# Performance work log

Hardware: AMD Instinct MI355X
Metric: run time of the kernel (lower is better)

The kernel has to match this reference:

```python
import jax, jax.numpy as jnp
import numpy as np

N = 1_000_000      # occupied voxels
GRID = 256         # voxel grid extent per axis
K = 27             # 3^3 kernel offsets
CIN, COUT = 2, 16


def _build_nbr_map(coords: np.ndarray) -> np.ndarray:
    """Kernel-offset neighbor map like MinkowskiEngine's kernel map.
    coords: [N,3] unique int voxel coords. Returns [N,K] int32, -1 = no neighbor.
    """
    key = (coords[:, 0] * GRID + coords[:, 1]) * GRID + coords[:, 2]
    order = np.argsort(key)
    skey = key[order]
    offsets = np.array([[dx, dy, dz]
                        for dx in (-1, 0, 1)
                        for dy in (-1, 0, 1)
                        for dz in (-1, 0, 1)], dtype=np.int64)
    nbr = np.full((coords.shape[0], K), -1, dtype=np.int32)
    for k in range(K):
        nc = coords + offsets[k]
        valid = np.all((nc >= 0) & (nc < GRID), axis=1)
        nkey = (nc[:, 0] * GRID + nc[:, 1]) * GRID + nc[:, 2]
        pos = np.clip(np.searchsorted(skey, nkey), 0, coords.shape[0] - 1)
        hit = valid & (skey[pos] == nkey)
        nbr[:, k] = np.where(hit, order[pos].astype(np.int32), -1)
    return nbr


def setup_inputs() -> dict:
    rng = np.random.default_rng(0)
    lin = rng.choice(GRID ** 3, size=N, replace=False)  # unique voxel ids
    coords = np.stack([lin // (GRID * GRID), (lin // GRID) % GRID, lin % GRID],
                      axis=1).astype(np.int64)
    nbr = _build_nbr_map(coords)
    key = jax.random.key(0)
    k1, k2 = jax.random.split(key)
    features = jax.random.normal(k1, (N, CIN), dtype=jnp.float32)
    # MinkowskiConvolution kernel: one [Cin,Cout] matrix per kernel offset, no bias
    kernel = jax.random.normal(k2, (K, CIN, COUT), dtype=jnp.float32) * 0.1
    return {"features": features, "kernel": kernel, "nbr_idx": jnp.asarray(nbr)}


def reference(features, kernel, nbr_idx):
    # gather-GEMM-scatter sparse conv: out[n] = sum_k W_k^T x[nbr(n,k)]
    mask = (nbr_idx >= 0)
    safe = jnp.maximum(nbr_idx, 0)
    gathered = features[safe]                              # [N,K,Cin]
    gathered = gathered * mask[..., None].astype(features.dtype)
    return jnp.einsum('nkc,kcd->nd', gathered, kernel)     # [N,Cout]
```

## Files before the change

### kernel.cpp

```cpp
#include <hip/hip_runtime.h>

#define K_OFF 27
#define CIN   2
#define COUT  16
#define BLK   256
#define CH    9

__global__ __launch_bounds__(BLK) void spconv_gather_kernel(
    const float* __restrict__ feats,
    const float* __restrict__ w,
    const int*   __restrict__ nbr,
    float*       __restrict__ out,
    int n_pts)
{
    __shared__ int s_nbr[BLK * K_OFF];

    const int tid     = threadIdx.x;
    const int lane    = tid & 63;
    const int wv      = tid >> 6;
    const int base_pt = blockIdx.x * BLK;
    const int wpt     = base_pt + wv * 64;

    int* sw = s_nbr + wv * (64 * K_OFF);
    const long long g0         = (long long)wpt * K_OFF;
    const long long total_ints = (long long)n_pts * K_OFF;

    int4*       sw4 = reinterpret_cast<int4*>(sw);
    const int4* g4  = reinterpret_cast<const int4*>(nbr + g0);
    #pragma unroll
    for (int j = 0; j < 7; ++j) {
        const int i = lane + j * 64;
        if (i < (64 * K_OFF) / 4) {
            const long long g = g0 + (long long)i * 4;
            sw4[i] = (g + 3 < total_ints) ? g4[i] : make_int4(-1, -1, -1, -1);
        }
    }
    asm volatile("s_waitcnt lgkmcnt(0)" ::: "memory");
    __builtin_amdgcn_wave_barrier();

    const float2* feats2 = reinterpret_cast<const float2*>(feats);
    const int row = lane * K_OFF;

    auto issue = [&](int kb, float2* f, float* m) {
        #pragma unroll
        for (int j = 0; j < CH; ++j) {
            const int idx = sw[row + kb + j];
            m[j] = (idx >= 0) ? 1.0f : 0.0f;
            f[j] = feats2[idx > 0 ? idx : 0];
        }
    };
    float acc[COUT];
    #pragma unroll
    for (int d = 0; d < COUT; ++d) acc[d] = 0.f;

    auto fma9 = [&](int kb, const float2* f, const float* m) {
        #pragma unroll
        for (int j = 0; j < CH; ++j) {
            const float fx = f[j].x * m[j];
            const float fy = f[j].y * m[j];
            const float* wk = w + (kb + j) * (CIN * COUT);
            #pragma unroll
            for (int d = 0; d < COUT; ++d) {
                acc[d] = fmaf(fx, wk[d],        acc[d]);
                acc[d] = fmaf(fy, wk[COUT + d], acc[d]);
            }
        }
    };

    float2 fA[CH], fB[CH];
    float  mA[CH], mB[CH];
    issue(0,  fA, mA);
    issue(CH, fB, mB);
    fma9(0, fA, mA);
    issue(2 * CH, fA, mA);
    fma9(CH, fB, mB);
    fma9(2 * CH, fA, mA);

    const int n = base_pt + tid;
    if (n < n_pts) {
        float4* o = reinterpret_cast<float4*>(out + (size_t)n * COUT);
        o[0] = make_float4(acc[0],  acc[1],  acc[2],  acc[3]);
        o[1] = make_float4(acc[4],  acc[5],  acc[6],  acc[7]);
        o[2] = make_float4(acc[8],  acc[9],  acc[10], acc[11]);
        o[3] = make_float4(acc[12], acc[13], acc[14], acc[15]);
    }
}

extern "C" void kernel_launch(void* const* d_in, const int* in_sizes, int n_in,
                              void* d_out, int out_size, void* d_ws, size_t ws_size,
                              hipStream_t stream) {
    const float* feats = (const float*)d_in[0];
    const float* w     = (const float*)d_in[1];
    const int*   nbr   = (const int*)d_in[2];
    float*       out   = (float*)d_out;

    const int n_pts = in_sizes[0] / CIN;
    const int grid  = (n_pts + BLK - 1) / BLK;

    spconv_gather_kernel<<<grid, BLK, 0, stream>>>(feats, w, nbr, out, n_pts);
}
```

Baseline: 64.02 us.

## Use persistent waves with register-prefetched neighbor tiles and two-chunk gather

Converts the kernel to a persistent grid capped at 1280 blocks, where each wave loops over 64-point tiles with a stride. It prefetches the next tile's neighbor indices into registers while the current tile is gathered and computed, so the index load overlaps with the feature gathers. The gather is also regrouped from three chunks of 9 into chunks of 14 and 13, which puts more loads in flight at a time. In exchange it raises register pressure and may lower occupancy, and the fixed grid cap may not suit every GPU configuration.

```diff
diff --git a/kernel.cpp b/kernel.cpp
--- a/kernel.cpp
+++ b/kernel.cpp
@@ -4,85 +4,127 @@
 #define CIN   2
 #define COUT  16
 #define BLK   256
-#define CH    9
+#define WAVES 4
+#define IPW   (64 * K_OFF)
+#define I4PW  (IPW / 4)
 
-__global__ __launch_bounds__(BLK) void spconv_gather_kernel(
+__global__ __launch_bounds__(BLK) void spconv_kernel(
     const float* __restrict__ feats,
     const float* __restrict__ w,
     const int*   __restrict__ nbr,
     float*       __restrict__ out,
-    int n_pts)
+    int n_pts, int n_tiles)
 {
-    __shared__ int s_nbr[BLK * K_OFF];
+    __shared__ int s_nbr[WAVES * IPW];
 
-    const int tid     = threadIdx.x;
-    const int lane    = tid & 63;
-    const int wv      = tid >> 6;
-    const int base_pt = blockIdx.x * BLK;
-    const int wpt     = base_pt + wv * 64;
+    const int tid  = threadIdx.x;
+    const int lane = tid & 63;
+    const int wv   = tid >> 6;
+    int* sw = s_nbr + wv * IPW;
+    int4* sw4 = reinterpret_cast<int4*>(sw);
 
-    int* sw = s_nbr + wv * (64 * K_OFF);
-    const long long g0         = (long long)wpt * K_OFF;
     const long long total_ints = (long long)n_pts * K_OFF;
+    const float2* feats2 = reinterpret_cast<const float2*>(feats);
 
-    int4*       sw4 = reinterpret_cast<int4*>(sw);
-    const int4* g4  = reinterpret_cast<const int4*>(nbr + g0);
-    #pragma unroll
-    for (int j = 0; j < 7; ++j) {
-        const int i = lane + j * 64;
-        if (i < (64 * K_OFF) / 4) {
+    const int wstride = gridDim.x * WAVES;
+    int tile = blockIdx.x * WAVES + wv;
+    if (tile >= n_tiles) return;
+
+    int4 r[7];
+    {
+        const long long g0 = (long long)tile * IPW;
+        const int4* g4 = reinterpret_cast<const int4*>(nbr + g0);
+        #pragma unroll
+        for (int j = 0; j < 7; ++j) {
+            const int i = lane + j * 64;
             const long long g = g0 + (long long)i * 4;
-            sw4[i] = (g + 3 < total_ints) ? g4[i] : make_int4(-1, -1, -1, -1);
+            r[j] = (i < I4PW && g + 3 < total_ints) ? g4[i] : make_int4(-1,-1,-1,-1);
         }
     }
-    asm volatile("s_waitcnt lgkmcnt(0)" ::: "memory");
-    __builtin_amdgcn_wave_barrier();
 
-    const float2* feats2 = reinterpret_cast<const float2*>(feats);
-    const int row = lane * K_OFF;
+    while (true) {
+        #pragma unroll
+        for (int j = 0; j < 7; ++j) {
+            const int i = lane + j * 64;
+            if (i < I4PW) sw4[i] = r[j];
+        }
+        asm volatile("s_waitcnt lgkmcnt(0)" ::: "memory");
+        __builtin_amdgcn_sched_barrier(0);
+        __builtin_amdgcn_wave_barrier();
 
-    auto issue = [&](int kb, float2* f, float* m) {
-        #pragma unroll
-        for (int j = 0; j < CH; ++j) {
-            const int idx = sw[row + kb + j];
-            m[j] = (idx >= 0) ? 1.0f : 0.0f;
-            f[j] = feats2[idx > 0 ? idx : 0];
-        }
-    };
-    float acc[COUT];
-    #pragma unroll
-    for (int d = 0; d < COUT; ++d) acc[d] = 0.f;
+        const int cur = tile;
+        tile += wstride;
+        const bool more = (tile < n_tiles);
 
-    auto fma9 = [&](int kb, const float2* f, const float* m) {
-        #pragma unroll
-        for (int j = 0; j < CH; ++j) {
-            const float fx = f[j].x * m[j];
-            const float fy = f[j].y * m[j];
-            const float* wk = w + (kb + j) * (CIN * COUT);
+        if (more) {
+            const long long g0 = (long long)tile * IPW;
+            const int4* g4 = reinterpret_cast<const int4*>(nbr + g0);
             #pragma unroll
-            for (int d = 0; d < COUT; ++d) {
-                acc[d] = fmaf(fx, wk[d],        acc[d]);
-                acc[d] = fmaf(fy, wk[COUT + d], acc[d]);
+            for (int j = 0; j < 7; ++j) {
+                const int i = lane + j * 64;
+                const long long g = g0 + (long long)i * 4;
+                r[j] = (i < I4PW && g + 3 < total_ints) ? g4[i] : make_int4(-1,-1,-1,-1);
             }
         }
-    };
 
-    float2 fA[CH], fB[CH];
-    float  mA[CH], mB[CH];
-    issue(0,  fA, mA);
-    issue(CH, fB, mB);
-    fma9(0, fA, mA);
-    issue(2 * CH, fA, mA);
-    fma9(CH, fB, mB);
-    fma9(2 * CH, fA, mA);
+        float acc[COUT];
+        #pragma unroll
+        for (int d = 0; d < COUT; ++d) acc[d] = 0.f;
+        const int row = lane * K_OFF;
 
-    const int n = base_pt + tid;
-    if (n < n_pts) {
-        float4* o = reinterpret_cast<float4*>(out + (size_t)n * COUT);
-        o[0] = make_float4(acc[0],  acc[1],  acc[2],  acc[3]);
-        o[1] = make_float4(acc[4],  acc[5],  acc[6],  acc[7]);
-        o[2] = make_float4(acc[8],  acc[9],  acc[10], acc[11]);
-        o[3] = make_float4(acc[12], acc[13], acc[14], acc[15]);
+        {
+            float2 f[14]; float m[14];
+            #pragma unroll
+            for (int j = 0; j < 14; ++j) {
+                const int idx = sw[row + j];
+                m[j] = (idx >= 0) ? 1.0f : 0.0f;
+                f[j] = feats2[idx > 0 ? idx : 0];
+            }
+            #pragma unroll
+            for (int j = 0; j < 14; ++j) {
+                const float fx = f[j].x * m[j];
+                const float fy = f[j].y * m[j];
+                const float* wk = w + j * (CIN * COUT);
+                #pragma unroll
+                for (int d = 0; d < COUT; ++d) {
+                    acc[d] = fmaf(fx, wk[d],        acc[d]);
+                    acc[d] = fmaf(fy, wk[COUT + d], acc[d]);
+                }
+            }
+        }
+        {
+            float2 f[13]; float m[13];
+            #pragma unroll
+            for (int j = 0; j < 13; ++j) {
+                const int idx = sw[row + 14 + j];
+                m[j] = (idx >= 0) ? 1.0f : 0.0f;
+                f[j] = feats2[idx > 0 ? idx : 0];
+            }
+            #pragma unroll
+            for (int j = 0; j < 13; ++j) {
+                const float fx = f[j].x * m[j];
+                const float fy = f[j].y * m[j];
+                const float* wk = w + (14 + j) * (CIN * COUT);
+                #pragma unroll
+                for (int d = 0; d < COUT; ++d) {
+                    acc[d] = fmaf(fx, wk[d],        acc[d]);
+                    acc[d] = fmaf(fy, wk[COUT + d], acc[d]);
+                }
+            }
+        }
+
+        const int n = cur * 64 + lane;
+        if (n < n_pts) {
+            float4* o = reinterpret_cast<float4*>(out + (size_t)n * COUT);
+            o[0] = make_float4(acc[0],  acc[1],  acc[2],  acc[3]);
+            o[1] = make_float4(acc[4],  acc[5],  acc[6],  acc[7]);
+            o[2] = make_float4(acc[8],  acc[9],  acc[10], acc[11]);
+            o[3] = make_float4(acc[12], acc[13], acc[14], acc[15]);
+        }
+
+        if (!more) break;
+        asm volatile("s_waitcnt lgkmcnt(0)" ::: "memory");
+        __builtin_amdgcn_wave_barrier();
     }
 }
 
@@ -94,8 +136,10 @@
     const int*   nbr   = (const int*)d_in[2];
     float*       out   = (float*)d_out;
 
-    const int n_pts = in_sizes[0] / CIN;
-    const int grid  = (n_pts + BLK - 1) / BLK;
+    const int n_pts   = in_sizes[0] / CIN;
+    const int n_tiles = (n_pts + 63) / 64;
+    int grid = (n_tiles + WAVES - 1) / WAVES;
+    if (grid > 1280) grid = 1280;
 
-    spconv_gather_kernel<<<grid, BLK, 0, stream>>>(feats, w, nbr, out, n_pts);
+    spconv_kernel<<<grid, BLK, 0, stream>>>(feats, w, nbr, out, n_pts, n_tiles);
 }
```

Result: no change. 64.61 us (+0.9%).
